# Kernel tuning notes

Hardware: AMD Instinct MI355X
Metric: run time of the kernel (lower is better)

## Reference

```python
import jax, jax.numpy as jnp
import numpy as np

EMBED_DIM = 1024
HEAD_DIM = 64


def setup_inputs() -> dict:
    key = jax.random.key(0)
    ks = jax.random.split(key, 7)
    B, S = 4, 2048
    s = 1.0 / np.sqrt(EMBED_DIM)
    h = jax.random.normal(ks[0], (B, S, EMBED_DIM), dtype=jnp.float32)
    Wq = jax.random.normal(ks[1], (EMBED_DIM, HEAD_DIM), dtype=jnp.float32) * s
    bq = jax.random.normal(ks[2], (HEAD_DIM,), dtype=jnp.float32) * 0.01
    Wk = jax.random.normal(ks[3], (EMBED_DIM, HEAD_DIM), dtype=jnp.float32) * s
    bk = jax.random.normal(ks[4], (HEAD_DIM,), dtype=jnp.float32) * 0.01
    Wv = jax.random.normal(ks[5], (EMBED_DIM, HEAD_DIM), dtype=jnp.float32) * s
    bv = jax.random.normal(ks[6], (HEAD_DIM,), dtype=jnp.float32) * 0.01
    return {"h": h, "Wq": Wq, "bq": bq, "Wk": Wk, "bk": bk, "Wv": Wv, "bv": bv}


def reference(h, Wq, bq, Wk, bk, Wv, bv):
    # Linear projections: h [B,S,E] -> q,k [B,S,D]
    q = jnp.einsum("bse,ed->bsd", h, Wq) + bq
    k = jnp.einsum("bse,ed->bsd", h, Wk) + bk
    v = jnp.einsum("bse,ed->bsd", h, Wv) + bv  # computed but UNUSED (faithful to source)
    del v
    scale = 1.0 / jnp.sqrt(jnp.asarray(HEAD_DIM, dtype=q.dtype))
    # scores [B, Sq, Sk]
    scores = jnp.einsum("bqd,bkd->bqk", q, k) * scale
    # NOTE: source uses softmax over dim=1 (query axis), not the key axis
    weights = jax.nn.softmax(scores, axis=1)
    # NOTE: source passes h (not v) as the value tensor
    out = jnp.einsum("bqk,bke->bqe", weights, h)  # [B, Sq, E]
    return out
```

## Files before the change

kernel.cpp:

```cpp
#include <hip/hip_runtime.h>
#include <hip/hip_bf16.h>
#include <math.h>

#define EMBED 1024
#define HDIM  64
#define BATCH 4
#define SEQ   2048

typedef __attribute__((ext_vector_type(8))) short short8;
typedef __attribute__((ext_vector_type(4))) float f32x4;
typedef unsigned int u32;
typedef unsigned short u16;

static __device__ __forceinline__ u16 f2bf(float f) {
    union { float f; u32 u; } v; v.f = f;
    u32 r = v.u + 0x7fffu + ((v.u >> 16) & 1u);
    return (u16)(r >> 16);
}

static __device__ __forceinline__ void gload_lds16(const u16* g, u16* l) {
    __builtin_amdgcn_global_load_lds(
        (const __attribute__((address_space(1))) u32*)g,
        (__attribute__((address_space(3))) u32*)l, 16, 0, 0);
}

__global__ __launch_bounds__(256) void wt_kernel(
    const float* __restrict__ Wq, const float* __restrict__ Wk,
    u16* __restrict__ WqT, u16* __restrict__ WkT)
{
    __shared__ float tile[64][65];
    const float* W = blockIdx.y ? Wk : Wq;
    u16* WT = blockIdx.y ? WkT : WqT;
    int e0 = blockIdx.x * 64;
    int t = threadIdx.x, c = t & 63, r4 = t >> 6;
    for (int r = r4; r < 64; r += 4)
        tile[r][c] = W[(size_t)(e0 + r) * HDIM + c];
    __syncthreads();
    for (int d = r4; d < 64; d += 4)
        WT[(size_t)d * EMBED + e0 + c] = f2bf(tile[c][d]);
}

__global__ __launch_bounds__(256) void proj_kernel(
    const float* __restrict__ h, const u16* __restrict__ WqT, const u16* __restrict__ WkT,
    const float* __restrict__ bq, const float* __restrict__ bk,
    u16* __restrict__ Qbf, u16* __restrict__ Kbf)
{
    __shared__ u16 hs[2][16][136];
    int b = blockIdx.x >> 7, s0 = (blockIdx.x & 127) * 16;
    int t = threadIdx.x, lane = t & 63, w = t >> 6;
    int l15 = lane & 15, quad = lane >> 4;
    int pj = w >> 1, nh = (w & 1) * 32;
    const float* hb = h + ((size_t)b * SEQ + s0) * EMBED;
    const u16* Wp = pj ? WkT : WqT;
    int r = t >> 4, c4 = (t & 15) * 4;

    f32x4 pre0 = *(const f32x4*)(hb + (size_t)r * EMBED + c4);
    f32x4 pre1 = *(const f32x4*)(hb + (size_t)r * EMBED + 64 + c4);
    f32x4 accA[2], accB[2];
    accA[0] = accA[1] = accB[0] = accB[1] = (f32x4){0.f, 0.f, 0.f, 0.f};

    const u16* Wrow0 = Wp + (size_t)(nh + l15) * EMBED;
    const u16* Wrow1 = Wp + (size_t)(nh + 16 + l15) * EMBED;

    short8 cw[8];
#pragma unroll
    for (int i = 0; i < 4; i++) {
        cw[i]     = *(const short8*)(Wrow0 + i * 32 + quad * 8);
        cw[4 + i] = *(const short8*)(Wrow1 + i * 32 + quad * 8);
    }

    for (int it = 0; it < 8; ++it) {
        int ec = it * 128, buf = it & 1;
        uint2 pk;
        pk.x = (u32)f2bf(pre0[0]) | ((u32)f2bf(pre0[1]) << 16);
        pk.y = (u32)f2bf(pre0[2]) | ((u32)f2bf(pre0[3]) << 16);
        *(uint2*)&hs[buf][r][c4] = pk;
        pk.x = (u32)f2bf(pre1[0]) | ((u32)f2bf(pre1[1]) << 16);
        pk.y = (u32)f2bf(pre1[2]) | ((u32)f2bf(pre1[3]) << 16);
        *(uint2*)&hs[buf][r][64 + c4] = pk;
        __syncthreads();

        if (it + 1 < 8) {
            pre0 = *(const f32x4*)(hb + (size_t)r * EMBED + ec + 128 + c4);
            pre1 = *(const f32x4*)(hb + (size_t)r * EMBED + ec + 192 + c4);
        }
        short8 nw[8];
#pragma unroll
        for (int i = 0; i < 8; i++) nw[i] = cw[i];
        if (it + 1 < 8) {
#pragma unroll
            for (int i = 0; i < 4; i++) {
                nw[i]     = *(const short8*)(Wrow0 + ec + 128 + i * 32 + quad * 8);
                nw[4 + i] = *(const short8*)(Wrow1 + ec + 128 + i * 32 + quad * 8);
            }
        }

        short8 a0 = *(const short8*)&hs[buf][l15][quad * 8];
        short8 a1 = *(const short8*)&hs[buf][l15][32 + quad * 8];
        short8 a2 = *(const short8*)&hs[buf][l15][64 + quad * 8];
        short8 a3 = *(const short8*)&hs[buf][l15][96 + quad * 8];
        accA[0] = __builtin_amdgcn_mfma_f32_16x16x32_bf16(a0, cw[0], accA[0], 0, 0, 0);
        accA[1] = __builtin_amdgcn_mfma_f32_16x16x32_bf16(a0, cw[4], accA[1], 0, 0, 0);
        accB[0] = __builtin_amdgcn_mfma_f32_16x16x32_bf16(a1, cw[1], accB[0], 0, 0, 0);
        accB[1] = __builtin_amdgcn_mfma_f32_16x16x32_bf16(a1, cw[5], accB[1], 0, 0, 0);
        accA[0] = __builtin_amdgcn_mfma_f32_16x16x32_bf16(a2, cw[2], accA[0], 0, 0, 0);
        accA[1] = __builtin_amdgcn_mfma_f32_16x16x32_bf16(a2, cw[6], accA[1], 0, 0, 0);
        accB[0] = __builtin_amdgcn_mfma_f32_16x16x32_bf16(a3, cw[3], accB[0], 0, 0, 0);
        accB[1] = __builtin_amdgcn_mfma_f32_16x16x32_bf16(a3, cw[7], accB[1], 0, 0, 0);
#pragma unroll
        for (int i = 0; i < 8; i++) cw[i] = nw[i];
    }

    const float* bias = pj ? bk : bq;
    float scale = pj ? 1.0f : 0.125f;
    u16* outp = pj ? Kbf : Qbf;
    float bv0 = bias[nh + l15], bv1 = bias[nh + 16 + l15];
#pragma unroll
    for (int rr = 0; rr < 4; rr++) {
        size_t row = (size_t)b * SEQ + s0 + quad * 4 + rr;
        outp[row * HDIM + nh + l15]      = f2bf((accA[0][rr] + accB[0][rr] + bv0) * scale);
        outp[row * HDIM + nh + 16 + l15] = f2bf((accA[1][rr] + accB[1][rr] + bv1) * scale);
    }
}

__global__ __launch_bounds__(256) void sw_kernel(
    const u16* __restrict__ Qbf, const u16* __restrict__ Kbf,
    u16* __restrict__ Wmat, float* __restrict__ invl)
{
    __shared__ float sl[4][16];
    int b = blockIdx.y;
    int k0 = blockIdx.x * 16;
    int t = threadIdx.x, lane = t & 63, w = t >> 6;
    int l15 = lane & 15, quad = lane >> 4;
    const u16* Qb = Qbf + (size_t)b * SEQ * HDIM;
    const u16* Kb = Kbf + (size_t)b * SEQ * HDIM;
    u16* Wb = Wmat + (size_t)b * SEQ * SEQ;
    short8 kf0 = *(const short8*)(Kb + (size_t)(k0 + l15) * HDIM + quad * 8);
    short8 kf1 = *(const short8*)(Kb + (size_t)(k0 + l15) * HDIM + 32 + quad * 8);
    f32x4 lacc = {0.f, 0.f, 0.f, 0.f};
    int qs = w * 512;
    const u16* qpa = Qb + (size_t)(qs + l15) * HDIM;
    const u16* qpb = Qb + (size_t)(qs + 16 + l15) * HDIM;
    short8 cf0a = *(const short8*)(qpa + quad * 8);
    short8 cf1a = *(const short8*)(qpa + 32 + quad * 8);
    short8 cf0b = *(const short8*)(qpb + quad * 8);
    short8 cf1b = *(const short8*)(qpb + 32 + quad * 8);

    for (int q0 = qs; q0 < qs + 512; q0 += 32) {
        short8 nf0a = cf0a, nf1a = cf1a, nf0b = cf0b, nf1b = cf1b;
        if (q0 + 32 < qs + 512) {
            const u16* na = Qb + (size_t)(q0 + 32 + l15) * HDIM;
            const u16* nb = Qb + (size_t)(q0 + 48 + l15) * HDIM;
            nf0a = *(const short8*)(na + quad * 8);
            nf1a = *(const short8*)(na + 32 + quad * 8);
            nf0b = *(const short8*)(nb + quad * 8);
            nf1b = *(const short8*)(nb + 32 + quad * 8);
        }
        f32x4 aa = {0.f, 0.f, 0.f, 0.f}, ab = {0.f, 0.f, 0.f, 0.f};
        aa = __builtin_amdgcn_mfma_f32_16x16x32_bf16(kf0, cf0a, aa, 0, 0, 0);
        ab = __builtin_amdgcn_mfma_f32_16x16x32_bf16(kf0, cf0b, ab, 0, 0, 0);
        aa = __builtin_amdgcn_mfma_f32_16x16x32_bf16(kf1, cf1a, aa, 0, 0, 0);
        ab = __builtin_amdgcn_mfma_f32_16x16x32_bf16(kf1, cf1b, ab, 0, 0, 0);
        float e0 = __expf(aa[0]), e1 = __expf(aa[1]);
        float e2 = __expf(aa[2]), e3 = __expf(aa[3]);
        float g0 = __expf(ab[0]), g1 = __expf(ab[1]);
        float g2 = __expf(ab[2]), g3 = __expf(ab[3]);
        lacc[0] += e0 + g0; lacc[1] += e1 + g1;
        lacc[2] += e2 + g2; lacc[3] += e3 + g3;
        uint2 pa, pb;
        pa.x = (u32)f2bf(e0) | ((u32)f2bf(e1) << 16);
        pa.y = (u32)f2bf(e2) | ((u32)f2bf(e3) << 16);
        pb.x = (u32)f2bf(g0) | ((u32)f2bf(g1) << 16);
        pb.y = (u32)f2bf(g2) | ((u32)f2bf(g3) << 16);
        *(uint2*)(Wb + (size_t)(q0 + l15) * SEQ + k0 + quad * 4) = pa;
        *(uint2*)(Wb + (size_t)(q0 + 16 + l15) * SEQ + k0 + quad * 4) = pb;
        cf0a = nf0a; cf1a = nf1a; cf0b = nf0b; cf1b = nf1b;
    }
#pragma unroll
    for (int m = 1; m <= 8; m <<= 1) {
        lacc[0] += __shfl_xor(lacc[0], m, 64);
        lacc[1] += __shfl_xor(lacc[1], m, 64);
        lacc[2] += __shfl_xor(lacc[2], m, 64);
        lacc[3] += __shfl_xor(lacc[3], m, 64);
    }
    if (l15 == 0) {
        sl[w][quad * 4 + 0] = lacc[0];
        sl[w][quad * 4 + 1] = lacc[1];
        sl[w][quad * 4 + 2] = lacc[2];
        sl[w][quad * 4 + 3] = lacc[3];
    }
    __syncthreads();
    if (t < 16)
        invl[b * SEQ + k0 + t] =
            1.0f / ((sl[0][t] + sl[1][t]) + (sl[2][t] + sl[3][t]));
}

__global__ __launch_bounds__(256) void tscale_kernel(
    const float* __restrict__ h, const float* __restrict__ invl,
    u16* __restrict__ hT)
{
    __shared__ float tile[64][65];
    int b  = blockIdx.z;
    int s0 = blockIdx.x * 64, e0 = blockIdx.y * 64;
    int t = threadIdx.x, c = t & 63, r4 = t >> 6;
    const float* hb = h + (size_t)b * SEQ * EMBED;
    for (int r = r4; r < 64; r += 4)
        tile[r][c] = hb[(size_t)(s0 + r) * EMBED + e0 + c];
    __syncthreads();
    float il = invl[b * SEQ + s0 + c];
    u16* hTb = hT + (size_t)b * EMBED * SEQ;
    for (int er = r4; er < 64; er += 4)
        hTb[(size_t)(e0 + er) * SEQ + s0 + c] = f2bf(tile[c][er] * il);
}

__global__ __launch_bounds__(256) void out_gemm_kernel(
    const u16* __restrict__ Wmat, const u16* __restrict__ hT, float* __restrict__ out)
{
    __shared__ u16 As[2][128 * 64];
    __shared__ u16 Bs[2][128 * 64];
    int b = blockIdx.z;
    int q0 = blockIdx.x * 128, e0 = blockIdx.y * 128;
    int t = threadIdx.x, lane = t & 63, w = t >> 6;
    int l15 = lane & 15, quad = lane >> 4;
    const u16* Wb  = Wmat + (size_t)b * SEQ * SEQ;
    const u16* hTb = hT + (size_t)b * EMBED * SEQ;
    int wq = (w & 1) * 64, we = (w >> 1) * 64;

    f32x4 acc[4][4];
#pragma unroll
    for (int qi = 0; qi < 4; qi++)
#pragma unroll
        for (int ei = 0; ei < 4; ei++) acc[qi][ei] = (f32x4){0.f, 0.f, 0.f, 0.f};

    int st_rl = lane >> 3;
    int st_pc = lane & 7;

#define STAGE(bi, k0)                                                          \
    {                                                                          \
        _Pragma("unroll")                                                      \
        for (int ld = 0; ld < 4; ld++) {                                       \
            int rowb = w * 32 + ld * 8;                                        \
            int row  = rowb + st_rl;                                           \
            int cg   = st_pc ^ (row & 7);            \
            gload_lds16(Wb  + (size_t)(q0 + row) * SEQ + (k0) + cg * 8,        \
                        &As[bi][rowb * 64] + lane * 8);                        \
            gload_lds16(hTb + (size_t)(e0 + row) * SEQ + (k0) + cg * 8,        \
                        &Bs[bi][rowb * 64] + lane * 8);                        \
        }                                                                      \
    }

    STAGE(0, 0)

    for (int it = 0; it < 32; ++it) {
        int buf = it & 1;
        __syncthreads();
        if (it + 1 < 32) STAGE(buf ^ 1, (it + 1) * 64)

        short8 af[2][4], bfr[2][4];
#pragma unroll
        for (int kf = 0; kf < 2; kf++)
#pragma unroll
            for (int i = 0; i < 4; i++) {
                int ra = wq + i * 16 + l15;
                int rb = we + i * 16 + l15;
                int pca = (kf * 4 + quad) ^ (ra & 7);
                int pcb = (kf * 4 + quad) ^ (rb & 7);
                af[kf][i]  = *(const short8*)(&As[buf][ra * 64] + pca * 8);
                bfr[kf][i] = *(const short8*)(&Bs[buf][rb * 64] + pcb * 8);
            }
#pragma unroll
        for (int kf = 0; kf < 2; kf++)
#pragma unroll
            for (int qi = 0; qi < 4; qi++)
#pragma unroll
                for (int ei = 0; ei < 4; ei++)
                    acc[qi][ei] = __builtin_amdgcn_mfma_f32_16x16x32_bf16(
                        af[kf][qi], bfr[kf][ei], acc[qi][ei], 0, 0, 0);
    }
#undef STAGE

    float* outb = out + (size_t)b * SEQ * EMBED;
#pragma unroll
    for (int qi = 0; qi < 4; qi++)
#pragma unroll
        for (int ei = 0; ei < 4; ei++)
#pragma unroll
            for (int r = 0; r < 4; r++)
                outb[(size_t)(q0 + wq + qi * 16 + quad * 4 + r) * EMBED
                     + e0 + we + ei * 16 + l15] = acc[qi][ei][r];
}

extern "C" void kernel_launch(void* const* d_in, const int* in_sizes, int n_in,
                              void* d_out, int out_size, void* d_ws, size_t ws_size,
                              hipStream_t stream) {
    (void)in_sizes; (void)n_in; (void)out_size; (void)ws_size;
    const float* h  = (const float*)d_in[0];
    const float* Wq = (const float*)d_in[1];
    const float* bq = (const float*)d_in[2];
    const float* Wk = (const float*)d_in[3];
    const float* bk = (const float*)d_in[4];
    float* out = (float*)d_out;

    char* ws = (char*)d_ws;
    u16*   Qbf  = (u16*)(ws);
    u16*   Kbf  = (u16*)(ws + (1ull << 20));
    u16*   hT   = (u16*)(ws + (2ull << 20));
    float* invl = (float*)(ws + (18ull << 20));
    u16*   WqT  = (u16*)(ws + (18ull << 20) + (128ull << 10));
    u16*   WkT  = (u16*)(ws + (18ull << 20) + (256ull << 10));
    u16*   Wmat = (u16*)(ws + (19ull << 20));

    hipLaunchKernelGGL(wt_kernel, dim3(16, 2), dim3(256), 0, stream, Wq, Wk, WqT, WkT);
    hipLaunchKernelGGL(proj_kernel, dim3(512), dim3(256), 0, stream,
                       h, WqT, WkT, bq, bk, Qbf, Kbf);
    hipLaunchKernelGGL(sw_kernel, dim3(128, 4), dim3(256), 0, stream,
                       Qbf, Kbf, Wmat, invl);
    hipLaunchKernelGGL(tscale_kernel, dim3(32, 16, 4), dim3(256), 0, stream,
                       h, invl, hT);
    hipLaunchKernelGGL(out_gemm_kernel, dim3(16, 8, 4), dim3(256), 0, stream,
                       Wmat, hT, out);
}
```

Baseline: 191.3 us.

## Enlarge out GEMM tile to 256x128 with 8 waves and triple-buffered LDS pipeline

The output GEMM moves from 128x128 tiles with 4 waves to 256x128 tiles with 8 waves, so each B tile loaded from hT is reused by twice as many rows. Double buffering becomes a 3-stage ring with prefetch two tiles ahead, explicit vmcnt waits and a raw s_barrier in place of __syncthreads. MFMA sections are wrapped in s_setprio to favour compute issue. LDS use grows to about 144KB per block and the grid halves to 256 blocks, which may reduce occupancy and CU coverage.

```diff
diff --git a/kernel.cpp b/kernel.cpp
--- a/kernel.cpp
+++ b/kernel.cpp
@@ -213,69 +213,93 @@
         hTb[(size_t)(e0 + er) * SEQ + s0 + c] = f2bf(tile[c][er] * il);
 }
 
-__global__ __launch_bounds__(256) void out_gemm_kernel(
+__global__ __launch_bounds__(512, 2) void out_gemm_kernel(
     const u16* __restrict__ Wmat, const u16* __restrict__ hT, float* __restrict__ out)
 {
-    __shared__ u16 As[2][128 * 64];
-    __shared__ u16 Bs[2][128 * 64];
+    __shared__ u16 As[3][256 * 64];
+    __shared__ u16 Bs[3][128 * 64];
     int b = blockIdx.z;
-    int q0 = blockIdx.x * 128, e0 = blockIdx.y * 128;
+    int q0 = blockIdx.x * 256, e0 = blockIdx.y * 128;
     int t = threadIdx.x, lane = t & 63, w = t >> 6;
     int l15 = lane & 15, quad = lane >> 4;
     const u16* Wb  = Wmat + (size_t)b * SEQ * SEQ;
     const u16* hTb = hT + (size_t)b * EMBED * SEQ;
-    int wq = (w & 1) * 64, we = (w >> 1) * 64;
+    int wm = w >> 1, wn = w & 1;
+    int wq = wm * 64, we = wn * 64;
 
     f32x4 acc[4][4];
 #pragma unroll
     for (int qi = 0; qi < 4; qi++)
 #pragma unroll
-        for (int ei = 0; ei < 4; ei++) acc[qi][ei] = (f32x4){0.f, 0.f, 0.f, 0.f};
+        for (int ej = 0; ej < 4; ej++) acc[qi][ej] = (f32x4){0.f, 0.f, 0.f, 0.f};
 
     int st_rl = lane >> 3;
     int st_pc = lane & 7;
 
-#define STAGE(bi, k0)                                                          \
+#define STAGE(si, k0)                                                          \
     {                                                                          \
         _Pragma("unroll")                                                      \
         for (int ld = 0; ld < 4; ld++) {                                       \
             int rowb = w * 32 + ld * 8;                                        \
             int row  = rowb + st_rl;                                           \
             int cg   = st_pc ^ (row & 7);            \
-            gload_lds16(Wb  + (size_t)(q0 + row) * SEQ + (k0) + cg * 8,        \
-                        &As[bi][rowb * 64] + lane * 8);                        \
+            gload_lds16(Wb + (size_t)(q0 + row) * SEQ + (k0) + cg * 8,         \
+                        &As[si][rowb * 64] + lane * 8);                        \
+        }                                                                      \
+        _Pragma("unroll")                                                      \
+        for (int ld = 0; ld < 2; ld++) {                                       \
+            int rowb = w * 16 + ld * 8;                                        \
+            int row  = rowb + st_rl;                                           \
+            int cg   = st_pc ^ (row & 7);                                      \
             gload_lds16(hTb + (size_t)(e0 + row) * SEQ + (k0) + cg * 8,        \
-                        &Bs[bi][rowb * 64] + lane * 8);                        \
+                        &Bs[si][rowb * 64] + lane * 8);                        \
         }                                                                      \
     }
 
     STAGE(0, 0)
-
-    for (int it = 0; it < 32; ++it) {
-        int buf = it & 1;
-        __syncthreads();
-        if (it + 1 < 32) STAGE(buf ^ 1, (it + 1) * 64)
-
-        short8 af[2][4], bfr[2][4];
+    STAGE(1, 64)
+
+    for (int kt = 0; kt < 32; ++kt) {
+        int s = kt % 3;
+        if (kt == 31) { asm volatile("s_waitcnt vmcnt(0)" ::: "memory"); }
+        else          { asm volatile("s_waitcnt vmcnt(6)" ::: "memory"); }
+        __builtin_amdgcn_s_barrier();
+        asm volatile("" ::: "memory");
+        if (kt + 2 < 32) {
+            int s2 = (kt + 2) % 3;
+            STAGE(s2, (kt + 2) * 64)
+        }
+        asm volatile("" ::: "memory");
+
+        const u16* Ab = &As[s][0];
+        const u16* Bb = &Bs[s][0];
+        short8 bfr[2][4], af[2][4];
 #pragma unroll
         for (int kf = 0; kf < 2; kf++)
 #pragma unroll
+            for (int j = 0; j < 4; j++) {
+                int rb  = we + j * 16 + l15;
+                int pcb = (kf * 4 + quad) ^ (rb & 7);
+                bfr[kf][j] = *(const short8*)(Bb + rb * 64 + pcb * 8);
+            }
+#pragma unroll
+        for (int kf = 0; kf < 2; kf++)
+#pragma unroll
             for (int i = 0; i < 4; i++) {
-                int ra = wq + i * 16 + l15;
-                int rb = we + i * 16 + l15;
+                int ra  = wq + i * 16 + l15;
                 int pca = (kf * 4 + quad) ^ (ra & 7);
-                int pcb = (kf * 4 + quad) ^ (rb & 7);
-                af[kf][i]  = *(const short8*)(&As[buf][ra * 64] + pca * 8);
-                bfr[kf][i] = *(const short8*)(&Bs[buf][rb * 64] + pcb * 8);
+                af[kf][i] = *(const short8*)(Ab + ra * 64 + pca * 8);
             }
+        __builtin_amdgcn_s_setprio(1);
 #pragma unroll
         for (int kf = 0; kf < 2; kf++)
 #pragma unroll
             for (int qi = 0; qi < 4; qi++)
 #pragma unroll
-                for (int ei = 0; ei < 4; ei++)
-                    acc[qi][ei] = __builtin_amdgcn_mfma_f32_16x16x32_bf16(
-                        af[kf][qi], bfr[kf][ei], acc[qi][ei], 0, 0, 0);
+                for (int ej = 0; ej < 4; ej++)
+                    acc[qi][ej] = __builtin_amdgcn_mfma_f32_16x16x32_bf16(
+                        af[kf][qi], bfr[kf][ej], acc[qi][ej], 0, 0, 0);
+        __builtin_amdgcn_s_setprio(0);
     }
 #undef STAGE
 
@@ -283,11 +307,11 @@
 #pragma unroll
     for (int qi = 0; qi < 4; qi++)
 #pragma unroll
-        for (int ei = 0; ei < 4; ei++)
+        for (int ej = 0; ej < 4; ej++)
 #pragma unroll
             for (int r = 0; r < 4; r++)
                 outb[(size_t)(q0 + wq + qi * 16 + quad * 4 + r) * EMBED
-                     + e0 + we + ei * 16 + l15] = acc[qi][ei][r];
+                     + e0 + we + ej * 16 + l15] = acc[qi][ej][r];
 }
 
 extern "C" void kernel_launch(void* const* d_in, const int* in_sizes, int n_in,
@@ -317,6 +341,6 @@
                        Qbf, Kbf, Wmat, invl);
     hipLaunchKernelGGL(tscale_kernel, dim3(32, 16, 4), dim3(256), 0, stream,
                        h, invl, hT);
-    hipLaunchKernelGGL(out_gemm_kernel, dim3(16, 8, 4), dim3(256), 0, stream,
+    hipLaunchKernelGGL(out_gemm_kernel, dim3(8, 8, 4), dim3(512), 0, stream,
                        Wmat, hT, out);
 }
```

Measured after the change: 183.8 us. 1.04x faster.
